# Kernel tuning notes

Hardware: AMD Instinct MI355X
Metric: run time of the kernel (lower is better)

## Reference

```python
import jax, jax.numpy as jnp
import numpy as np
from jax import lax


def _make_kernel():
    # enhance_n_suppress_5x5 contour kernels: (96, 5, 5), only 4 channels non-zero
    n = 5
    k = np.zeros((96, n, n), dtype=np.float32)
    k[10] = np.array([[0, 0, 1, 0, 0], [0, 0, 1, 0, 0], [-1, -1, 0, -1, -1],
                      [0, 0, 1, 0, 0], [0, 0, 1, 0, 0]], np.float32) / 8.0
    k[5] = np.array([[0, 0, -1, 0, 0], [0, 0, -1, 0, 0], [1, 1, 0, 1, 1],
                     [0, 0, -1, 0, 0], [0, 0, -1, 0, 0]], np.float32) / 8.0
    diag = np.array([[1, 0, 0, 0, -1], [0, 1, 0, -1, 0], [0, 0, 0, 0, 0],
                     [0, -1, 0, 1, 0], [-1, 0, 0, 0, 1]], np.float32) / 8.0
    k[54] = diag
    k[67] = diag
    return jnp.asarray(k)


def setup_inputs() -> dict:
    key = jax.random.key(0)
    x = jax.random.normal(key, (128, 55, 55, 96), dtype=jnp.float32)  # NHWC
    kernel = _make_kernel()  # (96, 5, 5)
    return {"x": x, "kernel": kernel}


def reference(x, kernel):
    # Depthwise 5x5 correlation per channel + residual (same math as the
    # python double loop of slice+batch_dot in the original layer).
    ch = x.shape[-1]
    # (96,5,5) -> HWIO depthwise kernel (5,5,1,96)
    k = jnp.transpose(kernel, (1, 2, 0))[:, :, None, :]
    y = lax.conv_general_dilated(
        x, k,
        window_strides=(1, 1),
        padding="SAME",
        dimension_numbers=("NHWC", "HWIO", "NHWC"),
        feature_group_count=ch,
    )
    return x + y
```

## Files before the change

### kernel.cpp

```cpp
#include <hip/hip_runtime.h>

#define NB 128
#define HW 55
#define IMG (HW * HW)
#define CH 96
#define GROUPS 24
#define TAPS 25
#define NPIX (NB * IMG)
#define RSTRIP 5
#define NSTRIP (HW / RSTRIP)
#define NWG (NB * NSTRIP)
#define SROWS (RSTRIP + 4)
#define GCHUNK 4
#define SLOTG 32
#define NXCD 8
#define BITEMS (RSTRIP * HW * GROUPS)
#define QTR (BITEMS / 4)
#define SPIX (RSTRIP * HW)
#define STAGEN (SROWS * HW)

typedef float v4f __attribute__((ext_vector_type(4)));


__global__ void repack_kernel(const float* __restrict__ k,
                              float4* __restrict__ wslot,
                              int2* __restrict__ dslot,
                              int* __restrict__ tapflag,
                              int* __restrict__ gact,
                              int* __restrict__ nga,
                              int* __restrict__ nspad,
                              int* __restrict__ amask) {
    __shared__ int s_ns[GROUPS];
    int g = threadIdx.x;
    if (g < GROUPS) {
        int ns = 0;
        for (int tap = 0; tap < TAPS; ++tap) {
            float w0 = k[(4 * g + 0) * TAPS + tap];
            float w1 = k[(4 * g + 1) * TAPS + tap];
            float w2 = k[(4 * g + 2) * TAPS + tap];
            float w3 = k[(4 * g + 3) * TAPS + tap];
            if (w0 != 0.f || w1 != 0.f || w2 != 0.f || w3 != 0.f) {
                int dh = tap / 5 - 2, dw = tap % 5 - 2;
                wslot[g * SLOTG + ns] = make_float4(w0, w1, w2, w3);
                dslot[g * SLOTG + ns] = make_int2(dh + 2, dw);
                ++ns;
            }
        }
        for (int s = ns; s < SLOTG; ++s) {
            wslot[g * SLOTG + s] = make_float4(0.f, 0.f, 0.f, 0.f);
            dslot[g * SLOTG + s] = make_int2(2, 0);
        }
        tapflag[g] = (ns > 0) ? 1 : 0;
        s_ns[g] = ns;
    }
    __syncthreads();
    if (threadIdx.x == 0) {
        int na = 0, m = 0, msk = 0;
        for (int gg = 0; gg < GROUPS; ++gg)
            if (s_ns[gg] > 0) {
                gact[na++] = gg;
                msk |= (1 << gg);
                m = m > s_ns[gg] ? m : s_ns[gg];
            }
        *nga = na;
        *nspad = (m + 7) & ~7;
        *amask = msk;
    }
}

__global__ __launch_bounds__(256) void tiled_kernel(const float* __restrict__ x,
                                                    const float4* __restrict__ wslot,
                                                    const int2* __restrict__ dslot,
                                                    const int* __restrict__ gact,
                                                    const int* __restrict__ p_nga,
                                                    const int* __restrict__ p_nspad,
                                                    const int* __restrict__ p_amask,
                                                    float* __restrict__ out) {
    __shared__ v4f s_x[GCHUNK * STAGEN];
    __shared__ v4f s_cv[GCHUNK * SPIX];
    __shared__ float4 s_w[GCHUNK * 8];
    __shared__ int s_d[GCHUNK * 8];

    const int q = NWG / NXCD, r = NWG % NXCD;
    int xcd = blockIdx.x & (NXCD - 1);
    int bidx = blockIdx.x >> 3;
    int swz = (xcd < r ? xcd * (q + 1) : r * (q + 1) + (xcd - r) * q) + bidx;

    const int n = swz / NSTRIP;
    const int strip = swz % NSTRIP;
    const int h0 = strip * RSTRIP;
    const int tid = threadIdx.x;
    const int nga = *p_nga;
    const int amask = *p_amask;
    const int nsb = (*p_nspad) >> 3;
    const int base_f4 = (n * IMG + h0 * HW) * GROUPS;
    const v4f* x4 = (const v4f*)x;
    v4f* o4 = (v4f*)out;

    int nchunk = (nga + GCHUNK - 1) / GCHUNK;
    if (nchunk < 1) nchunk = 1;
    const bool single = (nchunk == 1);

    for (int c = 0; c < nchunk; ++c) {
        const int c0 = c * GCHUNK;
        int cn = nga - c0;
        if (cn > GCHUNK) cn = GCHUNK;
        if (cn < 0) cn = 0;

        if (tid < cn * 8) {
            int ci = tid >> 3, s = tid & 7;
            int gg = gact[c0 + ci];
            s_w[tid] = wslot[gg * SLOTG + s];
            int2 dd = dslot[gg * SLOTG + s];
            s_d[tid] = (dd.x << 8) | (dd.y + 2);
        }
        const int stcnt = STAGEN * cn;
        const int wcn = HW * cn;
        const int sq = (stcnt + 3) >> 2;
        for (int jj = tid; jj < sq; jj += 256) {
            int idx[4];
            v4f val[4];
#pragma unroll
            for (int kq = 0; kq < 4; ++kq) {
                int i = jj + kq * sq;
                idx[kq] = -1;
                if (i < stcnt) {
                    int srow = i / wcn;
                    int rem2 = i - srow * wcn;
                    int pix = rem2 / cn;
                    int ci = rem2 - pix * cn;
                    int h = h0 - 2 + srow;
                    v4f v = {0.f, 0.f, 0.f, 0.f};
                    if ((unsigned)h < (unsigned)HW)
                        v = x4[(n * IMG + h * HW + pix) * GROUPS + gact[c0 + ci]];
                    idx[kq] = ci * STAGEN + srow * HW + pix;
                    val[kq] = v;
                }
            }
#pragma unroll
            for (int kq = 0; kq < 4; ++kq)
                if (idx[kq] >= 0) s_x[idx[kq]] = val[kq];
        }
        __syncthreads();

        const int acnt = cn * SPIX;
        for (int j = tid; j < acnt; j += 256) {
            int ci = j / SPIX;
            int pixrel = j - ci * SPIX;
            int rr = pixrel / HW;
            int pix = pixrel - rr * HW;
            const v4f* sxg = s_x + ci * STAGEN;
            v4f acc = {0.f, 0.f, 0.f, 0.f};
#pragma unroll
            for (int si = 0; si < 8; ++si) {
                int d = s_d[ci * 8 + si];
                int srow = rr + (d >> 8);
                int pix2 = pix + (d & 255) - 2;
                bool valid = (unsigned)pix2 < (unsigned)HW;
                float sc = valid ? 1.f : 0.f;
                int p2 = valid ? pix2 : 0;
                v4f xv = sxg[srow * HW + p2];
                float4 wv = s_w[ci * 8 + si];
                acc.x += (wv.x * sc) * xv.x;
                acc.y += (wv.y * sc) * xv.y;
                acc.z += (wv.z * sc) * xv.z;
                acc.w += (wv.w * sc) * xv.w;
            }
            for (int sb = 1; sb < nsb; ++sb) {
                int gg = gact[c0 + ci];
#pragma unroll
                for (int si = 0; si < 8; ++si) {
                    int s = sb * 8 + si;
                    int2 dd = dslot[gg * SLOTG + s];
                    int srow = rr + dd.x;
                    int pix2 = pix + dd.y;
                    bool valid = (unsigned)pix2 < (unsigned)HW;
                    float sc = valid ? 1.f : 0.f;
                    int p2 = valid ? pix2 : 0;
                    v4f xv = sxg[srow * HW + p2];
                    float4 wv = wslot[gg * SLOTG + s];
                    acc.x += (wv.x * sc) * xv.x;
                    acc.y += (wv.y * sc) * xv.y;
                    acc.z += (wv.z * sc) * xv.z;
                    acc.w += (wv.w * sc) * xv.w;
                }
            }
            s_cv[ci * SPIX + pixrel] = acc;
        }
        __syncthreads();

        for (int jj = tid; jj < QTR; jj += 256) {
            const int i0 = jj, i1 = jj + QTR, i2 = jj + 2 * QTR, i3 = jj + 3 * QTR;
            v4f a0 = x4[base_f4 + i0];
            v4f a1 = x4[base_f4 + i1];
            v4f a2 = x4[base_f4 + i2];
            v4f a3 = x4[base_f4 + i3];
#pragma unroll
            for (int kq = 0; kq < 4; ++kq) {
                const int i = jj + kq * QTR;
                v4f acc = kq == 0 ? a0 : kq == 1 ? a1 : kq == 2 ? a2 : a3;
                int pr = i / GROUPS;
                int gout = i - pr * GROUPS;
                bool act = (amask >> gout) & 1;
                int aidx = __popc(amask & ((1u << gout) - 1));
                int local = aidx - c0;
                bool inchunk = act & (local >= 0) & (local < cn);
                if (inchunk) acc += s_cv[local * SPIX + pr];
                if (single || inchunk || (c == 0 && !act))
                    __builtin_nontemporal_store(acc, &o4[base_f4 + i]);
            }
        }
        if (c + 1 < nchunk) __syncthreads();
    }
}

__global__ __launch_bounds__(256) void fallback_kernel(const float* __restrict__ x,
                                                       const float* __restrict__ kraw,
                                                       float* __restrict__ out) {
    int t = blockIdx.x * 256 + threadIdx.x;
    if (t >= NPIX * GROUPS) return;
    int g = t % GROUPS;
    int pixel = t / GROUPS;
    int rem = pixel % IMG;
    int h = rem / HW;
    int w = rem - h * HW;
    int base = pixel * CH + g * 4;
    const float4 xc = *reinterpret_cast<const float4*>(x + base);
    float4 acc = make_float4(xc.x, xc.y, xc.z, xc.w);
#pragma unroll
    for (int dh = -2; dh <= 2; ++dh)
#pragma unroll
        for (int dw = -2; dw <= 2; ++dw) {
            const int tap = (dh + 2) * 5 + (dw + 2);
            const bool valid = ((unsigned)(h + dh) < (unsigned)HW) &
                               ((unsigned)(w + dw) < (unsigned)HW);
            const float vs = valid ? 1.0f : 0.0f;
            const int off = valid ? (dh * HW * CH + dw * CH) : 0;
            const float4 xv = *reinterpret_cast<const float4*>(x + base + off);
            acc.x += (kraw[(g * 4 + 0) * TAPS + tap] * vs) * xv.x;
            acc.y += (kraw[(g * 4 + 1) * TAPS + tap] * vs) * xv.y;
            acc.z += (kraw[(g * 4 + 2) * TAPS + tap] * vs) * xv.z;
            acc.w += (kraw[(g * 4 + 3) * TAPS + tap] * vs) * xv.w;
        }
    *reinterpret_cast<float4*>(out + base) = acc;
}

extern "C" void kernel_launch(void* const* d_in, const int* in_sizes, int n_in,
                              void* d_out, int out_size, void* d_ws, size_t ws_size,
                              hipStream_t stream) {
    const float* x = (const float*)d_in[0];
    const float* k = (const float*)d_in[1];
    float* out = (float*)d_out;

    const size_t sz_wslot = (size_t)GROUPS * SLOTG * sizeof(float4);
    const size_t sz_dslot = (size_t)GROUPS * SLOTG * sizeof(int2);
    const size_t sz_flag = GROUPS * sizeof(int);
    const size_t sz_gact = GROUPS * sizeof(int);
    const size_t ws_need = sz_wslot + sz_dslot + sz_flag + sz_gact + 3 * sizeof(int);

    if (ws_size >= ws_need) {
        char* p = (char*)d_ws;
        float4* wslot = (float4*)p;  p += sz_wslot;
        int2* dslot = (int2*)p;      p += sz_dslot;
        int* tapflag = (int*)p;      p += sz_flag;
        int* gact = (int*)p;         p += sz_gact;
        int* nga = (int*)p;          p += sizeof(int);
        int* nspad = (int*)p;        p += sizeof(int);
        int* amask = (int*)p;

        repack_kernel<<<1, 64, 0, stream>>>(k, wslot, dslot, tapflag, gact,
                                            nga, nspad, amask);
        tiled_kernel<<<NWG, 256, 0, stream>>>(x, wslot, dslot, gact, nga, nspad,
                                              amask, out);
    } else {
        const int blocks = (NPIX * GROUPS) / 256;
        fallback_kernel<<<blocks, 256, 0, stream>>>(x, k, out);
    }
}
```

Before: 82.92 us.

## Copy inactive channel groups directly and write active results straight from compute

Inactive channel groups are now copied from input to output in an up-front pass. Active groups add the residual by starting the accumulator from the staged centre pixel and store their result directly to global memory. This drops the s_cv shared buffer, one barrier and the second pass that re-read all of x, so LDS use and global reads go down. Active-group stores become scattered 16-byte writes with a GROUPS stride, and the nontemporal hint on stores is dropped.

```diff
diff --git a/kernel.cpp b/kernel.cpp
--- a/kernel.cpp
+++ b/kernel.cpp
@@ -77,9 +77,9 @@
                                                     const int* __restrict__ p_amask,
                                                     float* __restrict__ out) {
     __shared__ v4f s_x[GCHUNK * STAGEN];
-    __shared__ v4f s_cv[GCHUNK * SPIX];
     __shared__ float4 s_w[GCHUNK * 8];
     __shared__ int s_d[GCHUNK * 8];
+    __shared__ int s_gg[GCHUNK];
 
     const int q = NWG / NXCD, r = NWG % NXCD;
     int xcd = blockIdx.x & (NXCD - 1);
@@ -97,16 +97,29 @@
     const v4f* x4 = (const v4f*)x;
     v4f* o4 = (v4f*)out;
 
+    for (int jj = tid; jj < QTR; jj += 256) {
+        v4f a0 = x4[base_f4 + jj];
+        v4f a1 = x4[base_f4 + jj + QTR];
+        v4f a2 = x4[base_f4 + jj + 2 * QTR];
+        v4f a3 = x4[base_f4 + jj + 3 * QTR];
+#pragma unroll
+        for (int kq = 0; kq < 4; ++kq) {
+            const int i = jj + kq * QTR;
+            const int gout = i % GROUPS;
+            if (!((amask >> gout) & 1)) {
+                v4f v = kq == 0 ? a0 : kq == 1 ? a1 : kq == 2 ? a2 : a3;
+                o4[base_f4 + i] = v;
+            }
+        }
+    }
+
     int nchunk = (nga + GCHUNK - 1) / GCHUNK;
-    if (nchunk < 1) nchunk = 1;
-    const bool single = (nchunk == 1);
-
     for (int c = 0; c < nchunk; ++c) {
         const int c0 = c * GCHUNK;
         int cn = nga - c0;
         if (cn > GCHUNK) cn = GCHUNK;
-        if (cn < 0) cn = 0;
-
+
+        if (tid < cn) s_gg[tid] = gact[c0 + tid];
         if (tid < cn * 8) {
             int ci = tid >> 3, s = tid & 7;
             int gg = gact[c0 + ci];
@@ -150,7 +163,7 @@
             int rr = pixrel / HW;
             int pix = pixrel - rr * HW;
             const v4f* sxg = s_x + ci * STAGEN;
-            v4f acc = {0.f, 0.f, 0.f, 0.f};
+            v4f acc = sxg[(rr + 2) * HW + pix];
 #pragma unroll
             for (int si = 0; si < 8; ++si) {
                 int d = s_d[ci * 8 + si];
@@ -167,7 +180,7 @@
                 acc.w += (wv.w * sc) * xv.w;
             }
             for (int sb = 1; sb < nsb; ++sb) {
-                int gg = gact[c0 + ci];
+                int gg = s_gg[ci];
 #pragma unroll
                 for (int si = 0; si < 8; ++si) {
                     int s = sb * 8 + si;
@@ -185,30 +198,7 @@
                     acc.w += (wv.w * sc) * xv.w;
                 }
             }
-            s_cv[ci * SPIX + pixrel] = acc;
-        }
-        __syncthreads();
-
-        for (int jj = tid; jj < QTR; jj += 256) {
-            const int i0 = jj, i1 = jj + QTR, i2 = jj + 2 * QTR, i3 = jj + 3 * QTR;
-            v4f a0 = x4[base_f4 + i0];
-            v4f a1 = x4[base_f4 + i1];
-            v4f a2 = x4[base_f4 + i2];
-            v4f a3 = x4[base_f4 + i3];
-#pragma unroll
-            for (int kq = 0; kq < 4; ++kq) {
-                const int i = jj + kq * QTR;
-                v4f acc = kq == 0 ? a0 : kq == 1 ? a1 : kq == 2 ? a2 : a3;
-                int pr = i / GROUPS;
-                int gout = i - pr * GROUPS;
-                bool act = (amask >> gout) & 1;
-                int aidx = __popc(amask & ((1u << gout) - 1));
-                int local = aidx - c0;
-                bool inchunk = act & (local >= 0) & (local < cn);
-                if (inchunk) acc += s_cv[local * SPIX + pr];
-                if (single || inchunk || (c == 0 && !act))
-                    __builtin_nontemporal_store(acc, &o4[base_f4 + i]);
-            }
+            o4[base_f4 + pixrel * GROUPS + s_gg[ci]] = acc;
         }
         if (c + 1 < nchunk) __syncthreads();
     }
```

After: 129.4 us. 1.56x slower.

## Store staged tiles in bf16 and pad columns to drop bounds checks

Applied to the files above, without the earlier changes.

Shared-memory staging of the input tile and the convolution result now stores bf16 pairs instead of fp32 vectors, halving LDS footprint and bandwidth. The input tile gains a two-column zero halo on each side, which removes per-tap column validity checks. The active group ids are cached in shared memory. This reduces LDS traffic and ALU work but adds pack/unpack conversions and introduces bf16 rounding error into the convolution term.

```diff
diff --git a/kernel.cpp b/kernel.cpp
--- a/kernel.cpp
+++ b/kernel.cpp
@@ -11,15 +11,35 @@
 #define NSTRIP (HW / RSTRIP)
 #define NWG (NB * NSTRIP)
 #define SROWS (RSTRIP + 4)
+#define PADW (HW + 4)
 #define GCHUNK 4
 #define SLOTG 32
 #define NXCD 8
 #define BITEMS (RSTRIP * HW * GROUPS)
 #define QTR (BITEMS / 4)
 #define SPIX (RSTRIP * HW)
-#define STAGEN (SROWS * HW)
+#define SXSTRIDE (SROWS * PADW)
 
 typedef float v4f __attribute__((ext_vector_type(4)));
+
+__device__ __forceinline__ unsigned bf16rne(float f) {
+    unsigned u = __builtin_bit_cast(unsigned, f);
+    return (u + 0x7FFFu + ((u >> 16) & 1u)) >> 16;
+}
+__device__ __forceinline__ uint2 pack4(v4f v) {
+    uint2 r;
+    r.x = bf16rne(v.x) | (bf16rne(v.y) << 16);
+    r.y = bf16rne(v.z) | (bf16rne(v.w) << 16);
+    return r;
+}
+__device__ __forceinline__ v4f unpack4(uint2 p) {
+    v4f v;
+    v.x = __builtin_bit_cast(float, p.x << 16);
+    v.y = __builtin_bit_cast(float, p.x & 0xFFFF0000u);
+    v.z = __builtin_bit_cast(float, p.y << 16);
+    v.w = __builtin_bit_cast(float, p.y & 0xFFFF0000u);
+    return v;
+}
 
 
 __global__ void repack_kernel(const float* __restrict__ k,
@@ -76,10 +96,11 @@
                                                     const int* __restrict__ p_nspad,
                                                     const int* __restrict__ p_amask,
                                                     float* __restrict__ out) {
-    __shared__ v4f s_x[GCHUNK * STAGEN];
-    __shared__ v4f s_cv[GCHUNK * SPIX];
+    __shared__ uint2 s_x[GCHUNK * SXSTRIDE];
+    __shared__ uint2 s_cv[GCHUNK * SPIX];
     __shared__ float4 s_w[GCHUNK * 8];
     __shared__ int s_d[GCHUNK * 8];
+    __shared__ int s_gg[GCHUNK];
 
     const int q = NWG / NXCD, r = NWG % NXCD;
     int xcd = blockIdx.x & (NXCD - 1);
@@ -107,6 +128,7 @@
         if (cn > GCHUNK) cn = GCHUNK;
         if (cn < 0) cn = 0;
 
+        if (tid < cn) s_gg[tid] = gact[c0 + tid];
         if (tid < cn * 8) {
             int ci = tid >> 3, s = tid & 7;
             int gg = gact[c0 + ci];
@@ -114,8 +136,8 @@
             int2 dd = dslot[gg * SLOTG + s];
             s_d[tid] = (dd.x << 8) | (dd.y + 2);
         }
-        const int stcnt = STAGEN * cn;
-        const int wcn = HW * cn;
+        const int stcnt = SROWS * PADW * cn;
+        const int wcn = PADW * cn;
         const int sq = (stcnt + 3) >> 2;
         for (int jj = tid; jj < sq; jj += 256) {
             int idx[4];
@@ -127,19 +149,20 @@
                 if (i < stcnt) {
                     int srow = i / wcn;
                     int rem2 = i - srow * wcn;
-                    int pix = rem2 / cn;
-                    int ci = rem2 - pix * cn;
+                    int pp = rem2 / cn;
+                    int ci = rem2 - pp * cn;
                     int h = h0 - 2 + srow;
+                    int w = pp - 2;
                     v4f v = {0.f, 0.f, 0.f, 0.f};
-                    if ((unsigned)h < (unsigned)HW)
-                        v = x4[(n * IMG + h * HW + pix) * GROUPS + gact[c0 + ci]];
-                    idx[kq] = ci * STAGEN + srow * HW + pix;
+                    if (((unsigned)h < (unsigned)HW) & ((unsigned)w < (unsigned)HW))
+                        v = x4[(n * IMG + h * HW + w) * GROUPS + gact[c0 + ci]];
+                    idx[kq] = ci * SXSTRIDE + srow * PADW + pp;
                     val[kq] = v;
                 }
             }
 #pragma unroll
             for (int kq = 0; kq < 4; ++kq)
-                if (idx[kq] >= 0) s_x[idx[kq]] = val[kq];
+                if (idx[kq] >= 0) s_x[idx[kq]] = pack4(val[kq]);
         }
         __syncthreads();
 
@@ -149,52 +172,45 @@
             int pixrel = j - ci * SPIX;
             int rr = pixrel / HW;
             int pix = pixrel - rr * HW;
-            const v4f* sxg = s_x + ci * STAGEN;
+            const uint2* sxg = s_x + ci * SXSTRIDE;
             v4f acc = {0.f, 0.f, 0.f, 0.f};
 #pragma unroll
             for (int si = 0; si < 8; ++si) {
                 int d = s_d[ci * 8 + si];
                 int srow = rr + (d >> 8);
-                int pix2 = pix + (d & 255) - 2;
-                bool valid = (unsigned)pix2 < (unsigned)HW;
-                float sc = valid ? 1.f : 0.f;
-                int p2 = valid ? pix2 : 0;
-                v4f xv = sxg[srow * HW + p2];
+                int col = pix + (d & 255);
+                v4f xv = unpack4(sxg[srow * PADW + col]);
                 float4 wv = s_w[ci * 8 + si];
-                acc.x += (wv.x * sc) * xv.x;
-                acc.y += (wv.y * sc) * xv.y;
-                acc.z += (wv.z * sc) * xv.z;
-                acc.w += (wv.w * sc) * xv.w;
+                acc.x += wv.x * xv.x;
+                acc.y += wv.y * xv.y;
+                acc.z += wv.z * xv.z;
+                acc.w += wv.w * xv.w;
             }
             for (int sb = 1; sb < nsb; ++sb) {
-                int gg = gact[c0 + ci];
+                int gg = s_gg[ci];
 #pragma unroll
                 for (int si = 0; si < 8; ++si) {
                     int s = sb * 8 + si;
                     int2 dd = dslot[gg * SLOTG + s];
                     int srow = rr + dd.x;
-                    int pix2 = pix + dd.y;
-                    bool valid = (unsigned)pix2 < (unsigned)HW;
-                    float sc = valid ? 1.f : 0.f;
-                    int p2 = valid ? pix2 : 0;
-                    v4f xv = sxg[srow * HW + p2];
+                    int col = pix + 2 + dd.y;
+                    v4f xv = unpack4(sxg[srow * PADW + col]);
                     float4 wv = wslot[gg * SLOTG + s];
-                    acc.x += (wv.x * sc) * xv.x;
-                    acc.y += (wv.y * sc) * xv.y;
-                    acc.z += (wv.z * sc) * xv.z;
-                    acc.w += (wv.w * sc) * xv.w;
+                    acc.x += wv.x * xv.x;
+                    acc.y += wv.y * xv.y;
+                    acc.z += wv.z * xv.z;
+                    acc.w += wv.w * xv.w;
                 }
             }
-            s_cv[ci * SPIX + pixrel] = acc;
+            s_cv[ci * SPIX + pixrel] = pack4(acc);
         }
         __syncthreads();
 
         for (int jj = tid; jj < QTR; jj += 256) {
-            const int i0 = jj, i1 = jj + QTR, i2 = jj + 2 * QTR, i3 = jj + 3 * QTR;
-            v4f a0 = x4[base_f4 + i0];
-            v4f a1 = x4[base_f4 + i1];
-            v4f a2 = x4[base_f4 + i2];
-            v4f a3 = x4[base_f4 + i3];
+            v4f a0 = x4[base_f4 + jj];
+            v4f a1 = x4[base_f4 + jj + QTR];
+            v4f a2 = x4[base_f4 + jj + 2 * QTR];
+            v4f a3 = x4[base_f4 + jj + 3 * QTR];
 #pragma unroll
             for (int kq = 0; kq < 4; ++kq) {
                 const int i = jj + kq * QTR;
@@ -205,7 +221,10 @@
                 int aidx = __popc(amask & ((1u << gout) - 1));
                 int local = aidx - c0;
                 bool inchunk = act & (local >= 0) & (local < cn);
-                if (inchunk) acc += s_cv[local * SPIX + pr];
+                if (inchunk) {
+                    v4f cv = unpack4(s_cv[local * SPIX + pr]);
+                    acc.x += cv.x; acc.y += cv.y; acc.z += cv.z; acc.w += cv.w;
+                }
                 if (single || inchunk || (c == 0 && !act))
                     __builtin_nontemporal_store(acc, &o4[base_f4 + i]);
             }
```

After: 91.19 us. +10.0%, slower.
